# Kernel optimization log

Measured on AMD Instinct MI355X. Metric: run time of the kernel, lower is better.

Reference implementation:

```python
import jax, jax.numpy as jnp
import numpy as np

NHEAD = 16
EPS = 1e-6

def _phi_norm(x):
    # phi = silu, then L2 normalize over last dim (torch F.normalize: x / max(||x||, eps))
    x = jax.nn.silu(x)
    n = jnp.linalg.norm(x, axis=-1, keepdims=True)
    return x / jnp.maximum(n, EPS)

def setup_inputs() -> dict:
    key = jax.random.key(0)
    k1, k2, k3 = jax.random.split(key, 3)
    B, M, N, D = 4, 1024, 2048, 1024
    q = jax.random.normal(k1, (B, M, D), dtype=jnp.float32)
    kv = jax.random.normal(k2, (B, N, D), dtype=jnp.float32)
    kv_mask = jax.random.bernoulli(k3, 0.1, (B, N))  # True = masked out
    return {"q": q, "kv": kv, "kv_mask": kv_mask}

def reference(q, kv, kv_mask):
    B, M, D = q.shape
    N = kv.shape[1]
    dh = D // NHEAD
    # [B, H, M, dh] / [B, H, N, dh]
    qh = q.reshape(B, M, NHEAD, dh).transpose(0, 2, 1, 3)
    kh = kv.reshape(B, N, NHEAD, dh).transpose(0, 2, 1, 3)
    vh = kh  # values are raw kv heads (no phi/norm)
    qh_n = _phi_norm(qh)
    kh_n = _phi_norm(kh)
    scores = jnp.einsum('bhmd,bhnd->bhmn', qh_n, kh_n) / jnp.sqrt(jnp.asarray(dh, qh_n.dtype))
    scores = jnp.where(kv_mask[:, None, None, :], -jnp.inf, scores)
    attn = jax.nn.softmax(scores.astype(jnp.float32), axis=-1).astype(scores.dtype)
    out = jnp.einsum('bhmn,bhnd->bhmd', attn, vh)
    return out.transpose(0, 2, 1, 3).reshape(B, M, D)
```

## Files before the change

kernel.cpp:

```cpp
#include <hip/hip_runtime.h>
#include <hip/hip_bf16.h>
#include <cmath>
#include <stdint.h>

#define B_ 4
#define M_ 1024
#define N_ 2048
#define D_ 1024
#define H_ 16
#define DH_ 64
#define QT 128
#define NT 64
#define PITCH 72

typedef __bf16 bf16_t;
typedef __attribute__((ext_vector_type(8))) __bf16 bf16x8;
typedef __attribute__((ext_vector_type(4))) float f32x4;

static __device__ __forceinline__ float silu_f(float x) {
  return x / (1.0f + __expf(-x));
}

__global__ __launch_bounds__(256) void prep_kernel(
    const float* __restrict__ kv, const int* __restrict__ kv_mask,
    bf16_t* __restrict__ kp, bf16_t* __restrict__ vt,
    unsigned long long* __restrict__ mb) {
  __shared__ __align__(16) bf16_t Lt[NT][PITCH];
  const int bx = blockIdx.x;
  const int hp = bx & 7;
  const int nt = (bx >> 3) & 31;
  const int b  = bx >> 8;
  const int n0 = nt * NT;
  const int tid = threadIdx.x;

  #pragma unroll
  for (int hi = 0; hi < 2; ++hi) {
    const int h = hp * 2 + hi;
    const size_t bh = (size_t)(b * H_ + h);
    {
      const int r = tid >> 2, c0 = (tid & 3) * 16;
      const float* src = kv + ((size_t)(b * N_ + n0 + r)) * D_ + h * DH_ + c0;
      union { float f[16]; float4 v4[4]; } raw;
      raw.v4[0] = *(const float4*)(src + 0);
      raw.v4[1] = *(const float4*)(src + 4);
      raw.v4[2] = *(const float4*)(src + 8);
      raw.v4[3] = *(const float4*)(src + 12);
      float sv[16];
      float ss = 0.f;
      #pragma unroll
      for (int i = 0; i < 16; ++i) { sv[i] = silu_f(raw.f[i]); ss += sv[i] * sv[i]; }
      ss += __shfl_xor(ss, 1); ss += __shfl_xor(ss, 2);
      const float inv = 1.0f / fmaxf(sqrtf(ss), 1e-6f);
      union { bf16_t bs[16]; uint4 u[2]; } pk;
      #pragma unroll
      for (int i = 0; i < 16; ++i) pk.bs[i] = (bf16_t)(sv[i] * inv);
      uint4* kdst = (uint4*)(kp + (bh * N_ + n0 + r) * DH_ + c0);
      kdst[0] = pk.u[0]; kdst[1] = pk.u[1];
      union { bf16_t bs[16]; uint4 u[2]; } pv;
      #pragma unroll
      for (int i = 0; i < 16; ++i) pv.bs[i] = (bf16_t)raw.f[i];
      uint4* ldst = (uint4*)&Lt[r][c0];
      ldst[0] = pv.u[0]; ldst[1] = pv.u[1];
    }
    __syncthreads();
    {
      const int d = tid >> 2, nc = (tid & 3) * 16;
      union { bf16_t bs[16]; uint4 u[2]; } pk;
      #pragma unroll
      for (int i = 0; i < 16; ++i) pk.bs[i] = Lt[nc + i][d];
      uint4* dst = (uint4*)(vt + (bh * DH_ + d) * N_ + n0 + nc);
      dst[0] = pk.u[0]; dst[1] = pk.u[1];
    }
    __syncthreads();
  }
  if (bx == 0 && tid < B_ * (N_ / 64)) {
    const int b2 = tid >> 5, tt = tid & 31;
    unsigned long long m = 0ull;
    for (int i = 0; i < 64; ++i)
      if (kv_mask[b2 * N_ + tt * 64 + i]) m |= (1ull << i);
    mb[tid] = m;
  }
}

__global__ __launch_bounds__(512, 4) void attn_kernel(
    const float* __restrict__ q, const bf16_t* __restrict__ kp,
    const bf16_t* __restrict__ vt, const unsigned long long* __restrict__ mb,
    float* __restrict__ out) {
  __shared__ __align__(16) bf16_t Qs[QT][PITCH];
  __shared__ __align__(16) bf16_t Ks[NT][PITCH];
  __shared__ __align__(16) bf16_t Vs[DH_][PITCH];
  __shared__ __align__(16) bf16_t Ps[8][16][PITCH];

  const int tid  = threadIdx.x;
  const int w    = tid >> 6;
  const int lane = tid & 63;
  const int l15  = lane & 15, quad = lane >> 4;
  const int bh   = blockIdx.x >> 3;
  const int m0   = (blockIdx.x & 7) * QT;
  const int b = bh >> 4, h = bh & 15;

  #pragma unroll
  for (int it = 0; it < 4; ++it) {
    const int row = it * 32 + (tid >> 4);
    const int c = tid & 15;
    float4 v = *(const float4*)(q + ((size_t)(b * M_ + m0 + row)) * D_ + h * DH_ + c * 4);
    float s0 = silu_f(v.x), s1 = silu_f(v.y), s2 = silu_f(v.z), s3 = silu_f(v.w);
    float ss = s0*s0 + s1*s1 + s2*s2 + s3*s3;
    ss += __shfl_xor(ss, 1); ss += __shfl_xor(ss, 2);
    ss += __shfl_xor(ss, 4); ss += __shfl_xor(ss, 8);
    const float inv = 1.0f / fmaxf(sqrtf(ss), 1e-6f);
    union { bf16_t bs[4]; uint2 u; } pk;
    pk.bs[0] = (bf16_t)(s0 * inv); pk.bs[1] = (bf16_t)(s1 * inv);
    pk.bs[2] = (bf16_t)(s2 * inv); pk.bs[3] = (bf16_t)(s3 * inv);
    *(uint2*)&Qs[row][c * 4] = pk.u;
  }
  __syncthreads();

  bf16x8 qa[2];
  #pragma unroll
  for (int kc = 0; kc < 2; ++kc)
    qa[kc] = *(const bf16x8*)&Qs[w * 16 + l15][kc * 32 + quad * 8];

  f32x4 o[4];
  float lrun[4];
  #pragma unroll
  for (int jd = 0; jd < 4; ++jd) o[jd] = (f32x4){0.f, 0.f, 0.f, 0.f};
  #pragma unroll
  for (int r = 0; r < 4; ++r) lrun[r] = 0.f;

  const bf16_t* kpb = kp + (size_t)bh * N_ * DH_;
  const bf16_t* vtb = vt + (size_t)bh * DH_ * N_;

  for (int t = 0; t < N_ / NT; ++t) {
    const int rr = tid >> 3, c8 = tid & 7;
    *(bf16x8*)&Ks[rr][c8 * 8] = *(const bf16x8*)(kpb + (size_t)(t * NT + rr) * DH_ + c8 * 8);
    *(bf16x8*)&Vs[rr][c8 * 8] = *(const bf16x8*)(vtb + (size_t)rr * N_ + t * NT + c8 * 8);
    __syncthreads();

    const unsigned long long mk = mb[b * (N_ / 64) + t];

    f32x4 s[4];
    #pragma unroll
    for (int j = 0; j < 4; ++j) s[j] = (f32x4){0.f, 0.f, 0.f, 0.f};
    #pragma unroll
    for (int kc = 0; kc < 2; ++kc)
      #pragma unroll
      for (int j = 0; j < 4; ++j) {
        bf16x8 kb = *(const bf16x8*)&Ks[j * 16 + l15][kc * 32 + quad * 8];
        s[j] = __builtin_amdgcn_mfma_f32_16x16x32_bf16(qa[kc], kb, s[j], 0, 0, 0);
      }

    float p[4][4];
    #pragma unroll
    for (int j = 0; j < 4; ++j) {
      const bool masked = (mk >> (l15 + 16 * j)) & 1ull;
      #pragma unroll
      for (int r = 0; r < 4; ++r) {
        const float e = __expf(s[j][r] * 0.125f - 0.125f);
        p[j][r] = masked ? 0.f : e;
      }
    }
    #pragma unroll
    for (int r = 0; r < 4; ++r)
      lrun[r] += (p[0][r] + p[1][r]) + (p[2][r] + p[3][r]);

    #pragma unroll
    for (int j = 0; j < 4; ++j)
      #pragma unroll
      for (int r = 0; r < 4; ++r)
        Ps[w][quad * 4 + r][l15 + 16 * j] = (bf16_t)p[j][r];

    #pragma unroll
    for (int kc = 0; kc < 2; ++kc) {
      bf16x8 pa = *(const bf16x8*)&Ps[w][l15][kc * 32 + quad * 8];
      #pragma unroll
      for (int jd = 0; jd < 4; ++jd) {
        bf16x8 vb = *(const bf16x8*)&Vs[jd * 16 + l15][kc * 32 + quad * 8];
        o[jd] = __builtin_amdgcn_mfma_f32_16x16x32_bf16(pa, vb, o[jd], 0, 0, 0);
      }
    }
    __syncthreads();
  }

  #pragma unroll
  for (int r = 0; r < 4; ++r) {
    lrun[r] += __shfl_xor(lrun[r], 1); lrun[r] += __shfl_xor(lrun[r], 2);
    lrun[r] += __shfl_xor(lrun[r], 4); lrun[r] += __shfl_xor(lrun[r], 8);
  }
  #pragma unroll
  for (int r = 0; r < 4; ++r) {
    const float lv = lrun[r];
    const float invl = lv > 0.f ? 1.0f / lv : 0.f;
    const int m = m0 + w * 16 + quad * 4 + r;
    const size_t base = ((size_t)(b * M_ + m)) * D_ + h * DH_ + l15;
    #pragma unroll
    for (int jd = 0; jd < 4; ++jd)
      out[base + jd * 16] = o[jd][r] * invl;
  }
}

extern "C" void kernel_launch(void* const* d_in, const int* in_sizes, int n_in,
                              void* d_out, int out_size, void* d_ws, size_t ws_size,
                              hipStream_t stream) {
  const float* q  = (const float*)d_in[0];
  const float* kv = (const float*)d_in[1];
  const int* kv_mask = (const int*)d_in[2];
  float* out = (float*)d_out;

  bf16_t* kp = (bf16_t*)d_ws;
  bf16_t* vt = kp + (size_t)B_ * H_ * N_ * DH_;
  unsigned long long* mb =
      (unsigned long long*)((char*)d_ws + 2 * (size_t)B_ * H_ * N_ * DH_ * sizeof(bf16_t));

  prep_kernel<<<B_ * 32 * 8, 256, 0, stream>>>(kv, kv_mask, kp, vt, mb);
  attn_kernel<<<B_ * H_ * (M_ / QT), 512, 0, stream>>>(q, kp, vt, mb, out);
}
```

Measured before the change: 170.4 us.

## Rewrite attention kernel with 32x32 MFMA, register P, and async double-buffered loads

Replaces the attention kernel with 4 waves that each own 32 query rows. QK^T and PV now use 32x32x16 bf16 MFMAs. The P tile stays in registers through v_permlane32_swap instead of round-tripping through LDS. K/V tiles are double-buffered via global_load_lds direct-to-LDS loads into an XOR-swizzled layout, and there is a single barrier per tile, s_setprio around the MFMA groups, exp2 with a folded scale, and a remapped block order for L2 locality. This is meant to cut LDS traffic, barriers and load latency, at the cost of more registers per thread, lower occupancy bounds and hardware-specific inline asm.

```diff
diff --git a/kernel.cpp b/kernel.cpp
--- a/kernel.cpp
+++ b/kernel.cpp
@@ -9,16 +9,33 @@
 #define D_ 1024
 #define H_ 16
 #define DH_ 64
-#define QT 128
 #define NT 64
+#define NTILES (N_ / NT)
 #define PITCH 72
 
 typedef __bf16 bf16_t;
 typedef __attribute__((ext_vector_type(8))) __bf16 bf16x8;
-typedef __attribute__((ext_vector_type(4))) float f32x4;
+typedef __attribute__((ext_vector_type(16))) float f32x16;
 
 static __device__ __forceinline__ float silu_f(float x) {
   return x / (1.0f + __expf(-x));
+}
+
+static __device__ __forceinline__ unsigned pk2(float a, float b) {
+  union { __bf16 h[2]; unsigned u; } p;
+  p.h[0] = (__bf16)a; p.h[1] = (__bf16)b;
+  return p.u;
+}
+
+static __device__ __forceinline__ void pl32swap(unsigned &x, unsigned &y) {
+  asm volatile("s_nop 0\n\tv_permlane32_swap_b32 %0, %1" : "+v"(x), "+v"(y));
+}
+
+static __device__ __forceinline__ void gload16(const bf16_t* g, bf16_t* l) {
+  typedef __attribute__((address_space(1))) const unsigned GU;
+  typedef __attribute__((address_space(3))) unsigned LU;
+  __builtin_amdgcn_global_load_lds((GU*)(const unsigned*)g, (LU*)(unsigned*)l,
+                                   16, 0, 0);
 }
 
 __global__ __launch_bounds__(256) void prep_kernel(
@@ -82,120 +99,166 @@
   }
 }
 
-__global__ __launch_bounds__(512, 4) void attn_kernel(
+__global__ __launch_bounds__(256, 2) void attn_kernel(
     const float* __restrict__ q, const bf16_t* __restrict__ kp,
     const bf16_t* __restrict__ vt, const unsigned long long* __restrict__ mb,
     float* __restrict__ out) {
-  __shared__ __align__(16) bf16_t Qs[QT][PITCH];
-  __shared__ __align__(16) bf16_t Ks[NT][PITCH];
-  __shared__ __align__(16) bf16_t Vs[DH_][PITCH];
-  __shared__ __align__(16) bf16_t Ps[8][16][PITCH];
+  __shared__ __align__(16) bf16_t Ksh[2][NT * DH_];
+  __shared__ __align__(16) bf16_t Vsh[2][DH_ * NT];
 
   const int tid  = threadIdx.x;
   const int w    = tid >> 6;
   const int lane = tid & 63;
-  const int l15  = lane & 15, quad = lane >> 4;
-  const int bh   = blockIdx.x >> 3;
-  const int m0   = (blockIdx.x & 7) * QT;
+  const int l31  = lane & 31;
+  const int hi   = lane >> 5;
+  const int rho  = l31 & 7;
+
+  const int wg = (blockIdx.x & 7) * 64 + (blockIdx.x >> 3);
+  const int bh = wg >> 3;
+  const int m0 = (wg & 7) * 128;
   const int b = bh >> 4, h = bh & 15;
-
-  #pragma unroll
-  for (int it = 0; it < 4; ++it) {
-    const int row = it * 32 + (tid >> 4);
-    const int c = tid & 15;
-    float4 v = *(const float4*)(q + ((size_t)(b * M_ + m0 + row)) * D_ + h * DH_ + c * 4);
-    float s0 = silu_f(v.x), s1 = silu_f(v.y), s2 = silu_f(v.z), s3 = silu_f(v.w);
-    float ss = s0*s0 + s1*s1 + s2*s2 + s3*s3;
-    ss += __shfl_xor(ss, 1); ss += __shfl_xor(ss, 2);
-    ss += __shfl_xor(ss, 4); ss += __shfl_xor(ss, 8);
-    const float inv = 1.0f / fmaxf(sqrtf(ss), 1e-6f);
-    union { bf16_t bs[4]; uint2 u; } pk;
-    pk.bs[0] = (bf16_t)(s0 * inv); pk.bs[1] = (bf16_t)(s1 * inv);
-    pk.bs[2] = (bf16_t)(s2 * inv); pk.bs[3] = (bf16_t)(s3 * inv);
-    *(uint2*)&Qs[row][c * 4] = pk.u;
-  }
-  __syncthreads();
-
-  bf16x8 qa[2];
-  #pragma unroll
-  for (int kc = 0; kc < 2; ++kc)
-    qa[kc] = *(const bf16x8*)&Qs[w * 16 + l15][kc * 32 + quad * 8];
-
-  f32x4 o[4];
-  float lrun[4];
-  #pragma unroll
-  for (int jd = 0; jd < 4; ++jd) o[jd] = (f32x4){0.f, 0.f, 0.f, 0.f};
-  #pragma unroll
-  for (int r = 0; r < 4; ++r) lrun[r] = 0.f;
 
   const bf16_t* kpb = kp + (size_t)bh * N_ * DH_;
   const bf16_t* vtb = vt + (size_t)bh * DH_ * N_;
 
-  for (int t = 0; t < N_ / NT; ++t) {
-    const int rr = tid >> 3, c8 = tid & 7;
-    *(bf16x8*)&Ks[rr][c8 * 8] = *(const bf16x8*)(kpb + (size_t)(t * NT + rr) * DH_ + c8 * 8);
-    *(bf16x8*)&Vs[rr][c8 * 8] = *(const bf16x8*)(vtb + (size_t)rr * N_ + t * NT + c8 * 8);
+  const int srow  = lane >> 3;
+  const int sslot = (lane & 7) ^ srow;
+  const bf16_t* ks0 = kpb + (size_t)(w * 16 + srow) * DH_ + sslot * 8;
+  const bf16_t* ks1 = ks0 + 8 * DH_;
+  const bf16_t* vs0 = vtb + (size_t)(w * 16 + srow) * N_ + sslot * 8;
+  const bf16_t* vs1 = vs0 + 8 * N_;
+
+  gload16(ks0, &Ksh[0][(w * 16) * DH_]);
+  gload16(ks1, &Ksh[0][(w * 16 + 8) * DH_]);
+  gload16(vs0, &Vsh[0][(w * 16) * NT]);
+  gload16(vs1, &Vsh[0][(w * 16 + 8) * NT]);
+
+  bf16x8 qb[4];
+  {
+    const float* qrow =
+        q + ((size_t)(b * M_ + m0 + w * 32 + l31)) * D_ + h * DH_ + hi * 8;
+    float sv[32];
+    float ss = 0.f;
+    #pragma unroll
+    for (int kk = 0; kk < 4; ++kk) {
+      float4 a0 = *(const float4*)(qrow + kk * 16);
+      float4 a1 = *(const float4*)(qrow + kk * 16 + 4);
+      sv[kk * 8 + 0] = silu_f(a0.x); sv[kk * 8 + 1] = silu_f(a0.y);
+      sv[kk * 8 + 2] = silu_f(a0.z); sv[kk * 8 + 3] = silu_f(a0.w);
+      sv[kk * 8 + 4] = silu_f(a1.x); sv[kk * 8 + 5] = silu_f(a1.y);
+      sv[kk * 8 + 6] = silu_f(a1.z); sv[kk * 8 + 7] = silu_f(a1.w);
+      #pragma unroll
+      for (int i = 0; i < 8; ++i) ss += sv[kk * 8 + i] * sv[kk * 8 + i];
+    }
+    ss += __shfl_xor(ss, 32);
+    const float inv = 1.0f / fmaxf(sqrtf(ss), 1e-6f);
+    #pragma unroll
+    for (int kk = 0; kk < 4; ++kk) {
+      union { unsigned u[4]; bf16x8 v; } pq;
+      #pragma unroll
+      for (int jj = 0; jj < 4; ++jj)
+        pq.u[jj] = pk2(sv[kk * 8 + jj * 2] * inv, sv[kk * 8 + jj * 2 + 1] * inv);
+      qb[kk] = pq.v;
+    }
+  }
+
+  int foff[2][4];
+  #pragma unroll
+  for (int i = 0; i < 2; ++i)
+    #pragma unroll
+    for (int j = 0; j < 4; ++j)
+      foff[i][j] = (i * 32 + l31) * 64 + ((((j << 1) + hi) ^ rho) << 3);
+
+  f32x16 o0, o1;
+  #pragma unroll
+  for (int r = 0; r < 16; ++r) { o0[r] = 0.f; o1[r] = 0.f; }
+  float lrun = 0.f;
+  const unsigned long long* mbb = mb + b * (N_ / 64);
+  const float C1 = 0.125f * 1.44269504f;
+
+  for (int t = 0; t < NTILES; ++t) {
     __syncthreads();
-
-    const unsigned long long mk = mb[b * (N_ / 64) + t];
-
-    f32x4 s[4];
-    #pragma unroll
-    for (int j = 0; j < 4; ++j) s[j] = (f32x4){0.f, 0.f, 0.f, 0.f};
-    #pragma unroll
-    for (int kc = 0; kc < 2; ++kc)
-      #pragma unroll
-      for (int j = 0; j < 4; ++j) {
-        bf16x8 kb = *(const bf16x8*)&Ks[j * 16 + l15][kc * 32 + quad * 8];
-        s[j] = __builtin_amdgcn_mfma_f32_16x16x32_bf16(qa[kc], kb, s[j], 0, 0, 0);
-      }
-
-    float p[4][4];
-    #pragma unroll
-    for (int j = 0; j < 4; ++j) {
-      const bool masked = (mk >> (l15 + 16 * j)) & 1ull;
-      #pragma unroll
-      for (int r = 0; r < 4; ++r) {
-        const float e = __expf(s[j][r] * 0.125f - 0.125f);
-        p[j][r] = masked ? 0.f : e;
-      }
-    }
-    #pragma unroll
-    for (int r = 0; r < 4; ++r)
-      lrun[r] += (p[0][r] + p[1][r]) + (p[2][r] + p[3][r]);
-
-    #pragma unroll
-    for (int j = 0; j < 4; ++j)
-      #pragma unroll
-      for (int r = 0; r < 4; ++r)
-        Ps[w][quad * 4 + r][l15 + 16 * j] = (bf16_t)p[j][r];
-
-    #pragma unroll
-    for (int kc = 0; kc < 2; ++kc) {
-      bf16x8 pa = *(const bf16x8*)&Ps[w][l15][kc * 32 + quad * 8];
-      #pragma unroll
-      for (int jd = 0; jd < 4; ++jd) {
-        bf16x8 vb = *(const bf16x8*)&Vs[jd * 16 + l15][kc * 32 + quad * 8];
-        o[jd] = __builtin_amdgcn_mfma_f32_16x16x32_bf16(pa, vb, o[jd], 0, 0, 0);
-      }
-    }
-    __syncthreads();
-  }
-
-  #pragma unroll
-  for (int r = 0; r < 4; ++r) {
-    lrun[r] += __shfl_xor(lrun[r], 1); lrun[r] += __shfl_xor(lrun[r], 2);
-    lrun[r] += __shfl_xor(lrun[r], 4); lrun[r] += __shfl_xor(lrun[r], 8);
-  }
-  #pragma unroll
-  for (int r = 0; r < 4; ++r) {
-    const float lv = lrun[r];
-    const float invl = lv > 0.f ? 1.0f / lv : 0.f;
-    const int m = m0 + w * 16 + quad * 4 + r;
-    const size_t base = ((size_t)(b * M_ + m)) * D_ + h * DH_ + l15;
-    #pragma unroll
-    for (int jd = 0; jd < 4; ++jd)
-      out[base + jd * 16] = o[jd][r] * invl;
+    const int cur = t & 1;
+    if (t + 1 < NTILES) {
+      const int nxt = cur ^ 1;
+      const size_t ko = (size_t)(t + 1) * NT * DH_;
+      const size_t vo = (size_t)(t + 1) * NT;
+      gload16(ks0 + ko, &Ksh[nxt][(w * 16) * DH_]);
+      gload16(ks1 + ko, &Ksh[nxt][(w * 16 + 8) * DH_]);
+      gload16(vs0 + vo, &Vsh[nxt][(w * 16) * NT]);
+      gload16(vs1 + vo, &Vsh[nxt][(w * 16 + 8) * NT]);
+    }
+    const unsigned long long mk = mbb[t];
+    const bf16_t* Kc = Ksh[cur];
+    const bf16_t* Vc = Vsh[cur];
+
+    bf16x8 pa[4];
+    #pragma unroll
+    for (int nb = 0; nb < 2; ++nb) {
+      f32x16 s;
+      #pragma unroll
+      for (int r = 0; r < 16; ++r) s[r] = 0.f;
+      __builtin_amdgcn_s_setprio(1);
+      #pragma unroll
+      for (int kk = 0; kk < 4; ++kk) {
+        bf16x8 ka = *(const bf16x8*)(Kc + foff[nb][kk]);
+        s = __builtin_amdgcn_mfma_f32_32x32x16_bf16(ka, qb[kk], s, 0, 0, 0);
+      }
+      __builtin_amdgcn_s_setprio(0);
+
+      const unsigned um = (unsigned)(mk >> (nb * 32 + (hi << 2)));
+      float p[16];
+      #pragma unroll
+      for (int r = 0; r < 16; ++r) {
+        const float e = exp2f(s[r] * C1 - C1);
+        p[r] = ((um >> ((r & 3) + ((r >> 2) << 3))) & 1u) ? 0.f : e;
+      }
+      lrun += (((p[0] + p[1]) + (p[2] + p[3])) + ((p[4] + p[5]) + (p[6] + p[7]))) +
+              (((p[8] + p[9]) + (p[10] + p[11])) + ((p[12] + p[13]) + (p[14] + p[15])));
+
+      unsigned pkw[4][2];
+      #pragma unroll
+      for (int qq = 0; qq < 4; ++qq) {
+        pkw[qq][0] = pk2(p[qq * 4 + 0], p[qq * 4 + 1]);
+        pkw[qq][1] = pk2(p[qq * 4 + 2], p[qq * 4 + 3]);
+      }
+      #pragma unroll
+      for (int tt = 0; tt < 2; ++tt) {
+        union { unsigned u[4]; bf16x8 v; } fr;
+        #pragma unroll
+        for (int ww = 0; ww < 2; ++ww) {
+          const unsigned own = hi ? pkw[2 * tt + 1][ww] : pkw[2 * tt][ww];
+          unsigned x = hi ? pkw[2 * tt][ww] : pkw[2 * tt + 1][ww];
+          unsigned y = x;
+          pl32swap(x, y);
+          fr.u[ww]     = hi ? x : own;
+          fr.u[2 + ww] = hi ? own : y;
+        }
+        pa[nb * 2 + tt] = fr.v;
+      }
+    }
+
+    __builtin_amdgcn_s_setprio(1);
+    #pragma unroll
+    for (int ks = 0; ks < 4; ++ks) {
+      bf16x8 vb0 = *(const bf16x8*)(Vc + foff[0][ks]);
+      bf16x8 vb1 = *(const bf16x8*)(Vc + foff[1][ks]);
+      o0 = __builtin_amdgcn_mfma_f32_32x32x16_bf16(pa[ks], vb0, o0, 0, 0, 0);
+      o1 = __builtin_amdgcn_mfma_f32_32x32x16_bf16(pa[ks], vb1, o1, 0, 0, 0);
+    }
+    __builtin_amdgcn_s_setprio(0);
+  }
+
+  lrun += __shfl_xor(lrun, 32);
+  #pragma unroll
+  for (int r = 0; r < 16; ++r) {
+    const int mrow = (r & 3) + ((r >> 2) << 3) + (hi << 2);
+    const float lv = __shfl(lrun, mrow);
+    const float iv = lv > 0.f ? 1.0f / lv : 0.f;
+    const size_t base =
+        ((size_t)(b * M_ + m0 + w * 32 + mrow)) * D_ + h * DH_ + l31;
+    out[base]      = o0[r] * iv;
+    out[base + 32] = o1[r] * iv;
   }
 }
 
@@ -213,5 +276,5 @@
       (unsigned long long*)((char*)d_ws + 2 * (size_t)B_ * H_ * N_ * DH_ * sizeof(bf16_t));
 
   prep_kernel<<<B_ * 32 * 8, 256, 0, stream>>>(kv, kv_mask, kp, vt, mb);
-  attn_kernel<<<B_ * H_ * (M_ / QT), 512, 0, stream>>>(q, kp, vt, mb, out);
-}
+  attn_kernel<<<B_ * H_ * (M_ / 128), 256, 0, stream>>>(q, kp, vt, mb, out);
+}
```

Result: slower. 178.3 us (+4.7%).
